# Kernel optimization log

Measured on AMD Instinct MI355X. Metric: run time of the kernel, lower is better.

Reference implementation:

```python
import jax, jax.numpy as jnp
import numpy as np

LO = 30            # rollout horizon (hard-coded in SimCore)
AS_DIM = 400       # ssbm_actionstate_dim
HEAD = AS_DIM + 7  # per-player decoder width


def setup_inputs() -> dict:
    key = jax.random.key(0)
    ks = jax.random.split(key, 12)
    T, B, A, H = 128, 256, 64, 1024
    Nt, Ng = 6, 4
    Lu = T - 1 - LO
    s = 0.02
    return dict(
        observations=jax.random.uniform(ks[0], (T, B, 16), jnp.float32),
        actions=jax.random.normal(ks[1], (T, B, A), jnp.float32),
        beliefs=jax.random.normal(ks[2], (T, B, H), jnp.float32),
        w_ih=jax.random.normal(ks[3], (3 * H, A), jnp.float32) * s,
        w_hh=jax.random.normal(ks[4], (3 * H, H), jnp.float32) * s,
        b_ih=jnp.zeros((3 * H,), jnp.float32),
        b_hh=jnp.zeros((3 * H,), jnp.float32),
        pre_w1=jax.random.normal(ks[5], (64, H), jnp.float32) * s,
        pre_b1=jnp.zeros((64,), jnp.float32),
        pre_w2=jax.random.normal(ks[6], (H, 64), jnp.float32) * s,
        pre_b2=jnp.zeros((H,), jnp.float32),
        dec_w=jax.random.normal(ks[7], (2 * HEAD, H), jnp.float32) * s,
        dec_b=jnp.zeros((2 * HEAD,), jnp.float32),
        idx_i=jax.random.randint(ks[8], (Nt,), 0, Lu, dtype=jnp.int32),
        K=jax.random.randint(ks[9], (Nt, Ng), 0, LO, dtype=jnp.int32),
    )


def _bce_logits(x, t):
    # binary_cross_entropy_with_logits, elementwise
    return jax.nn.softplus(x) - x * t


def _player_loss(pred, tgt):
    # pred: [Nt,Ng,B,407] logits; tgt: [Nt,Ng,B,8] observation half
    # pytorch means are over everything except the Nt python loop -> mean over (Ng,B[,feat])
    logits = pred[..., :AS_DIM]
    cls = tgt[..., 0].astype(jnp.int32)                     # .long() of float target
    ce = -jnp.take_along_axis(jax.nn.log_softmax(logits, -1), cls[..., None], -1)[..., 0]
    loss = ce.mean(axis=(1, 2))
    loss = loss + ((pred[..., 400:402] - tgt[..., 1:3]) ** 2).mean(axis=(1, 2, 3))
    loss = loss + ((jax.nn.softplus(pred[..., 402:403]) - tgt[..., 3:4]) ** 2).mean(axis=(1, 2, 3))
    loss = loss + ((jax.nn.softplus(pred[..., 403:404]) - tgt[..., 4:5]) ** 2).mean(axis=(1, 2, 3))
    loss = loss + _bce_logits(pred[..., 404:405], tgt[..., 5:6]).mean(axis=(1, 2, 3))
    loss = loss + _bce_logits(pred[..., 405:406], tgt[..., 6:7]).mean(axis=(1, 2, 3))
    loss = loss + _bce_logits(pred[..., 406:407], tgt[..., 7:8]).mean(axis=(1, 2, 3))
    return loss  # [Nt]


def reference(observations, actions, beliefs, w_ih, w_hh, b_ih, b_hh,
              pre_w1, pre_b1, pre_w2, pre_b2, dec_w, dec_b, idx_i, K):
    def gru_cell(h, a):
        gi = a @ w_ih.T + b_ih              # [B,3H]
        gh = h @ w_hh.T + b_hh
        ir, iz, in_ = jnp.split(gi, 3, axis=-1)
        hr, hz, hn = jnp.split(gh, 3, axis=-1)
        r = jax.nn.sigmoid(ir + hr)
        z = jax.nn.sigmoid(iz + hz)
        n = jnp.tanh(in_ + r * hn)
        h_new = (1.0 - z) * n + z * h
        return h_new, h_new

    def rollout(i, k):
        h0 = beliefs[i]                                          # [B,H]
        acts = jax.lax.dynamic_slice_in_dim(actions, i, LO, axis=0)
        _, states = jax.lax.scan(gru_cell, h0, acts)             # [Lo,B,H]
        return states[k], observations[k + i + 1]                # [Ng,B,H],[Ng,B,16]

    states, obs = jax.vmap(rollout)(idx_i, K)                    # [Nt,Ng,B,H]

    # ResidualBlock: x + relu(relu(x W1^T + b1) W2^T + b2)
    h = jax.nn.relu(states @ pre_w1.T + pre_b1)
    x = states + jax.nn.relu(h @ pre_w2.T + pre_b2)

    logits = x @ dec_w.T + dec_b                                 # [Nt,Ng,B,814]
    agent, opponent = logits[..., :HEAD], logits[..., HEAD:]
    tgt_a, tgt_o = obs[..., :8], obs[..., 8:]

    loss = (_player_loss(agent, tgt_a) + _player_loss(opponent, tgt_o)).sum()
    return loss
```

## Files before the change

### kernel.cpp

```cpp
#include <hip/hip_runtime.h>
#include <hip/hip_bf16.h>

typedef __bf16 bf16;
typedef __attribute__((ext_vector_type(4))) __bf16 bf16x4;
typedef __attribute__((ext_vector_type(8))) __bf16 bf16x8;
typedef __attribute__((ext_vector_type(4))) float f32x4;

static __device__ __forceinline__ f32x4 MFMA(bf16x8 a, bf16x8 b, f32x4 c) {
  return __builtin_amdgcn_mfma_f32_16x16x32_bf16(a, b, c, 0, 0, 0);
}

__device__ __forceinline__ float sigm(float x) { return 1.0f / (1.0f + __expf(-x)); }
__device__ __forceinline__ float softplus_(float x) {
  return fmaxf(x, 0.0f) + log1pf(__expf(-fabsf(x)));
}

__device__ __forceinline__ void gl16(const bf16* g, char* l) {
  __builtin_amdgcn_global_load_lds(
      (const __attribute__((address_space(1))) char*)g,
      (__attribute__((address_space(3))) char*)l, 16, 0, 0);
}

__global__ void k_prep(const float* __restrict__ whh, const float* __restrict__ wih,
                       const float* __restrict__ act, const float* __restrict__ w1,
                       const float* __restrict__ w2, const float* __restrict__ dw,
                       const float* __restrict__ beliefs, const int* __restrict__ idx_i,
                       bf16* __restrict__ Whd, bf16* __restrict__ Wid,
                       bf16* __restrict__ actd, bf16* __restrict__ w1d,
                       bf16* __restrict__ w2d, bf16* __restrict__ dwd,
                       bf16* __restrict__ hAd) {
  for (int q = blockIdx.x * blockDim.x + threadIdx.x; q < 1994240;
       q += gridDim.x * blockDim.x) {
    const float* src;
    bf16* dst;
    int off;
    if (q < 786432)       { src = whh; dst = Whd;  off = q; }
    else if (q < 835584)  { src = wih; dst = Wid;  off = q - 786432; }
    else if (q < 1359872) { src = act; dst = actd; off = q - 835584; }
    else if (q < 1376256) { src = w1;  dst = w1d;  off = q - 1359872; }
    else if (q < 1392640) { src = w2;  dst = w2d;  off = q - 1376256; }
    else if (q < 1601024) { src = dw;  dst = dwd;  off = q - 1392640; }
    else {
      const int e = (q - 1601024) << 2;
      const int n = e >> 18, rest = e & 262143;
      float4 v = *(const float4*)&beliefs[((size_t)idx_i[n] << 18) + rest];
      bf16x4 o = {(bf16)v.x, (bf16)v.y, (bf16)v.z, (bf16)v.w};
      *(bf16x4*)&hAd[e] = o;
      continue;
    }
    float4 v = *(const float4*)&src[(size_t)off << 2];
    bf16x4 o = {(bf16)v.x, (bf16)v.y, (bf16)v.z, (bf16)v.w};
    *(bf16x4*)&dst[(size_t)off << 2] = o;
  }
}

__global__ __launch_bounds__(256, 2) void k_gru_step(
    const bf16* __restrict__ hin, bf16* __restrict__ hout,
    const bf16* __restrict__ Wh, const bf16* __restrict__ Wi,
    const bf16* __restrict__ actB,
    const float* __restrict__ b_ih, const float* __restrict__ b_hh,
    const int* __restrict__ idx_i, const int* __restrict__ Kmat,
    bf16* __restrict__ states, int step) {
  const int pid = blockIdx.x;
  const int xcd = pid & 7;
  const int rg = xcd >> 2;
  const int cgp = xcd & 3;
  const int q = pid >> 3;
  const int mtl = q & 7;
  const int jtl = q >> 3;
  const int m0 = rg * 768 + mtl * 96;
  const int j0 = (cgp * 8 + jtl) * 32;

  {
    const int nlo = m0 >> 8, nhi = (m0 + 95) >> 8;
    int mk = Kmat[nlo * 4 + 0];
    mk = max(mk, Kmat[nlo * 4 + 1]);
    mk = max(mk, Kmat[nlo * 4 + 2]);
    mk = max(mk, Kmat[nlo * 4 + 3]);
    if (nhi != nlo) {
      mk = max(mk, Kmat[nhi * 4 + 0]);
      mk = max(mk, Kmat[nhi * 4 + 1]);
      mk = max(mk, Kmat[nhi * 4 + 2]);
      mk = max(mk, Kmat[nhi * 4 + 3]);
    }
    if (step > mk) return;
  }

  const int tid = threadIdx.x, wave = tid >> 6, lane = tid & 63;
  const int l15 = lane & 15;
  const int kgrp = lane >> 4;
  const int wm = wave >> 1;
  const int wj = wave & 1;
  const int jlane = j0 + wj * 16 + l15;

  __shared__ alignas(16) bf16 As[3][96][64];
  __shared__ alignas(16) bf16 Bs[3][96][64];

  const int srow = lane >> 3;
  const int scol = (((lane & 7) ^ srow) << 3);

  const bf16* asrc[3];
  const bf16* bsrc[3];
  const bf16* aisrc[3];
  const bf16* bisrc[3];
#pragma unroll
  for (int i = 0; i < 3; ++i) {
    const int prow = wave * 24 + i * 8 + srow;
    const int grow = m0 + prow;
    asrc[i] = hin + (size_t)grow * 1024 + scol;
    const int wr = (prow >> 5) * 1024 + j0 + (prow & 31);
    bsrc[i] = Wh + (size_t)wr * 1024 + scol;
    bisrc[i] = Wi + (size_t)wr * 64 + scol;
    const int np = grow >> 8;
    aisrc[i] = actB + ((size_t)(idx_i[np] + step) * 256 + (grow & 255)) * 64 + scol;
  }

  auto stage = [&](int buf, int it) {
    char* ad = (char*)As + buf * 12288 + (wave * 24) * 128;
    char* bd = (char*)Bs + buf * 12288 + (wave * 24) * 128;
    if (it < 16) {
#pragma unroll
      for (int i = 0; i < 3; ++i) {
        gl16(asrc[i] + it * 64, ad + i * 1024);
        gl16(bsrc[i] + it * 64, bd + i * 1024);
      }
    } else {
#pragma unroll
      for (int i = 0; i < 3; ++i) {
        gl16(aisrc[i], ad + i * 1024);
        gl16(bisrc[i], bd + i * 1024);
      }
    }
  };

  f32x4 accR[3], accZ[3], accNh[3], accNi[3];
  const f32x4 zero = {0.f, 0.f, 0.f, 0.f};
#pragma unroll
  for (int f = 0; f < 3; ++f) { accR[f] = zero; accZ[f] = zero; accNh[f] = zero; accNi[f] = zero; }

  const float br = b_ih[jlane] + b_hh[jlane];
  const float bz = b_ih[1024 + jlane] + b_hh[1024 + jlane];
  const float bin = b_ih[2048 + jlane];
  const float bhn = b_hh[2048 + jlane];

  auto compute = [&](int buf, f32x4 (&gN)[3]) {
    const char* ab = (const char*)As + buf * 12288;
    const char* bb = (const char*)Bs + buf * 12288;
#pragma unroll
    for (int kkI = 0; kkI < 2; ++kkI) {
      const int kbyte = (((kkI << 5) + (kgrp << 3)) << 1) ^ ((l15 & 7) << 4);
      bf16x8 a0 = *(const bf16x8*)(ab + (wm * 48 + l15) * 128 + kbyte);
      bf16x8 a1 = *(const bf16x8*)(ab + (wm * 48 + 16 + l15) * 128 + kbyte);
      bf16x8 a2 = *(const bf16x8*)(ab + (wm * 48 + 32 + l15) * 128 + kbyte);
      bf16x8 b_r = *(const bf16x8*)(bb + (wj * 16 + l15) * 128 + kbyte);
      bf16x8 b_z = *(const bf16x8*)(bb + (32 + wj * 16 + l15) * 128 + kbyte);
      bf16x8 b_n = *(const bf16x8*)(bb + (64 + wj * 16 + l15) * 128 + kbyte);
      accR[0] = MFMA(a0, b_r, accR[0]);
      accR[1] = MFMA(a1, b_r, accR[1]);
      accR[2] = MFMA(a2, b_r, accR[2]);
      accZ[0] = MFMA(a0, b_z, accZ[0]);
      accZ[1] = MFMA(a1, b_z, accZ[1]);
      accZ[2] = MFMA(a2, b_z, accZ[2]);
      gN[0] = MFMA(a0, b_n, gN[0]);
      gN[1] = MFMA(a1, b_n, gN[1]);
      gN[2] = MFMA(a2, b_n, gN[2]);
    }
  };

  stage(0, 0);
  stage(1, 1);

  uint2 hpreg[3];

#pragma unroll
  for (int t = 0; t < 17; ++t) {
    if (t < 15) stage((t + 2) % 3, t + 2);
    if (t == 14) {
#pragma unroll
      for (int it2 = 0; it2 < 3; ++it2) {
        const int u = it2 * 256 + tid;
        const int row = u >> 3, c = u & 7;
        hpreg[it2] = *(const uint2*)(hin + (size_t)(m0 + row) * 1024 + j0 + c * 4);
      }
    }
    if (t <= 13)      asm volatile("s_waitcnt vmcnt(12)" ::: "memory");
    else if (t == 14) asm volatile("s_waitcnt vmcnt(15)" ::: "memory");
    else if (t == 15) asm volatile("s_waitcnt vmcnt(9)" ::: "memory");
    else              asm volatile("s_waitcnt vmcnt(0)" ::: "memory");
    __builtin_amdgcn_s_barrier();
    if (t == 16) compute(1, accNi);
    else         compute(t % 3, accNh);
    __builtin_amdgcn_sched_barrier(0);
    __builtin_amdgcn_s_barrier();
  }

  bf16* Hp = (bf16*)&As[0][0][0];
  bf16* Hn = (bf16*)&Bs[0][0][0];

#pragma unroll
  for (int it2 = 0; it2 < 3; ++it2) {
    const int u = it2 * 256 + tid;
    const int row = u >> 3, c = u & 7;
    *(uint2*)&Hp[row * 40 + c * 4] = hpreg[it2];
  }
  __syncthreads();

#pragma unroll
  for (int mf = 0; mf < 3; ++mf) {
#pragma unroll
    for (int ii = 0; ii < 4; ++ii) {
      const int ml = wm * 48 + mf * 16 + kgrp * 4 + ii;
      const int jl = wj * 16 + l15;
      float hp = (float)Hp[ml * 40 + jl];
      float rg2 = sigm(accR[mf][ii] + br);
      float zg = sigm(accZ[mf][ii] + bz);
      float ng = tanhf(accNi[mf][ii] + bin + rg2 * (accNh[mf][ii] + bhn));
      float hnew = (1.0f - zg) * ng + zg * hp;
      Hn[ml * 40 + jl] = (bf16)hnew;
    }
  }
  __syncthreads();

#pragma unroll
  for (int it2 = 0; it2 < 3; ++it2) {
    const int u = it2 * 256 + tid;
    const int row = u >> 3, c = u & 7;
    const int m = m0 + row;
    uint2 v = *(const uint2*)&Hn[row * 40 + c * 4];
    *(uint2*)&hout[(size_t)m * 1024 + j0 + c * 4] = v;
    const int n = m >> 8;
    const int b = m & 255;
#pragma unroll
    for (int g = 0; g < 4; ++g) {
      if (Kmat[n * 4 + g] == step)
        *(uint2*)&states[((size_t)(n * 4 + g) * 256 + b) * 1024 + j0 + c * 4] = v;
    }
  }
}

template <int EPI, int SWZ>
__global__ __launch_bounds__(256) void k_gemm_epi(
    const bf16* __restrict__ A, const bf16* __restrict__ W, int K, int Nreal, int ld_out,
    const float* __restrict__ bias, const bf16* __restrict__ resid,
    float* __restrict__ outF, bf16* __restrict__ outB) {
  int mt, jt;
  if (SWZ) {
    const int lin = blockIdx.x;
    const int x = lin & 7, k = lin >> 3;
    mt = 12 * x + k % 12;
    jt = k / 12;
  } else {
    mt = blockIdx.x;
    jt = blockIdx.y;
  }
  const int m0 = mt * 64;
  const int j0 = jt * 64;
  const int tid = threadIdx.x, wave = tid >> 6, lane = tid & 63;
  __shared__ alignas(16) bf16 Al[64][72];
  __shared__ alignas(16) bf16 Wl[64][72];

  f32x4 acc[4];
  const f32x4 zero = {0.f, 0.f, 0.f, 0.f};
#pragma unroll
  for (int f = 0; f < 4; ++f) acc[f] = zero;

  const int r = tid >> 3, c8 = (tid & 7) << 3;
  const int arow = wave * 16 + (lane & 15);
  const int koff = (lane >> 4) << 3;

  for (int kb = 0; kb < K; kb += 64) {
    *(bf16x8*)&Al[r][c8]      = *(const bf16x8*)&A[(size_t)(m0 + r) * K + kb + c8];
    *(bf16x8*)&Al[r + 32][c8] = *(const bf16x8*)&A[(size_t)(m0 + r + 32) * K + kb + c8];
    int jr = j0 + r;      if (jr >= Nreal) jr = Nreal - 1;
    int jr2 = j0 + r + 32; if (jr2 >= Nreal) jr2 = Nreal - 1;
    *(bf16x8*)&Wl[r][c8]      = *(const bf16x8*)&W[(size_t)jr * K + kb + c8];
    *(bf16x8*)&Wl[r + 32][c8] = *(const bf16x8*)&W[(size_t)jr2 * K + kb + c8];
    __syncthreads();
#pragma unroll
    for (int kk = 0; kk < 64; kk += 32) {
      bf16x8 av = *(const bf16x8*)&Al[arow][kk + koff];
#pragma unroll
      for (int nf = 0; nf < 4; ++nf) {
        acc[nf] = MFMA(av, *(const bf16x8*)&Wl[nf * 16 + (lane & 15)][kk + koff], acc[nf]);
      }
    }
    __syncthreads();
  }

#pragma unroll
  for (int nf = 0; nf < 4; ++nf) {
    int j = j0 + nf * 16 + (lane & 15);
    float bj = (j < Nreal) ? bias[j] : 0.f;
#pragma unroll
    for (int i = 0; i < 4; ++i) {
      int m = m0 + wave * 16 + ((lane >> 4) << 2) + i;
      float v = acc[nf][i] + bj;
      if (EPI == 0) {
        outB[(size_t)m * ld_out + j] = (bf16)fmaxf(v, 0.f);
      } else if (EPI == 1) {
        v = fmaxf(v, 0.f) + (float)resid[(size_t)m * ld_out + j];
        outB[(size_t)m * ld_out + j] = (bf16)v;
      } else {
        if (j < Nreal) outF[(size_t)m * ld_out + j] = v;
      }
    }
  }
}

__global__ __launch_bounds__(256) void k_loss_wave(
    const float* __restrict__ logits, const float* __restrict__ obs,
    const int* __restrict__ idx_i, const int* __restrict__ Kmat,
    float* __restrict__ partials) {
  const int gw = blockIdx.x * 4 + (threadIdx.x >> 6);
  const int lane = threadIdx.x & 63;
  const int row = gw >> 1, p = gw & 1;
  const int n = row >> 10, g = (row >> 8) & 3, b = row & 255;
  const int i = idx_i[n], k = Kmat[n * 4 + g];
  const float* Lp = logits + (size_t)row * 814 + p * 407;
  const float* tg = obs + ((size_t)(k + i + 1) * 256 + b) * 16 + p * 8;

  float v[7];
#pragma unroll
  for (int it = 0; it < 7; ++it) {
    const int c = lane + it * 64;
    v[it] = (c < 400) ? Lp[c] : -1e30f;
  }
  float mx = fmaxf(fmaxf(fmaxf(v[0], v[1]), fmaxf(v[2], v[3])),
                   fmaxf(fmaxf(v[4], v[5]), v[6]));
#pragma unroll
  for (int s = 32; s; s >>= 1) mx = fmaxf(mx, __shfl_xor(mx, s));
  float se = 0.f;
#pragma unroll
  for (int it = 0; it < 7; ++it) {
    const int c = lane + it * 64;
    se += (c < 400) ? __expf(v[it] - mx) : 0.f;
  }
#pragma unroll
  for (int s = 32; s; s >>= 1) se += __shfl_xor(se, s);

  if (lane == 0) {
    const int cls = (int)tg[0];
    float val = mx + logf(se) - Lp[cls];
    const float d0 = Lp[400] - tg[1], d1 = Lp[401] - tg[2];
    val += 0.5f * (d0 * d0 + d1 * d1);
    const float s2 = softplus_(Lp[402]) - tg[3]; val += s2 * s2;
    const float s3 = softplus_(Lp[403]) - tg[4]; val += s3 * s3;
    val += softplus_(Lp[404]) - Lp[404] * tg[5];
    val += softplus_(Lp[405]) - Lp[405] * tg[6];
    val += softplus_(Lp[406]) - Lp[406] * tg[7];
    partials[gw] = val * (1.0f / 1024.0f);
  }
}

__global__ void k_reduce_final(const float* __restrict__ partials, float* __restrict__ out) {
  __shared__ float s[256];
  float v = 0.f;
  for (int i = threadIdx.x; i < 12288; i += 256) v += partials[i];
  s[threadIdx.x] = v;
  __syncthreads();
  for (int st = 128; st; st >>= 1) {
    if (threadIdx.x < st) s[threadIdx.x] += s[threadIdx.x + st];
    __syncthreads();
  }
  if (threadIdx.x == 0) out[0] = s[0];
}


extern "C" void kernel_launch(void* const* d_in, const int* in_sizes, int n_in,
                              void* d_out, int out_size, void* d_ws, size_t ws_size,
                              hipStream_t stream) {
  const float* obs      = (const float*)d_in[0];
  const float* actions  = (const float*)d_in[1];
  const float* beliefs  = (const float*)d_in[2];
  const float* w_ih     = (const float*)d_in[3];
  const float* w_hh     = (const float*)d_in[4];
  const float* b_ih     = (const float*)d_in[5];
  const float* b_hh     = (const float*)d_in[6];
  const float* pre_w1   = (const float*)d_in[7];
  const float* pre_b1   = (const float*)d_in[8];
  const float* pre_w2   = (const float*)d_in[9];
  const float* pre_b2   = (const float*)d_in[10];
  const float* dec_w    = (const float*)d_in[11];
  const float* dec_b    = (const float*)d_in[12];
  const int*   idx_i    = (const int*)d_in[13];
  const int*   Kmat     = (const int*)d_in[14];
  float* outF = (float*)d_out;

  char* p = (char*)d_ws;
  auto carve = [&](size_t bytes) {
    char* q = p;
    p += (bytes + 255) & ~(size_t)255;
    return q;
  };
  bf16* Wh      = (bf16*)carve(3072u * 1024u * 2u);
  bf16* Wi      = (bf16*)carve(3072u * 64u * 2u);
  bf16* actBv   = (bf16*)carve(128u * 256u * 64u * 2u);
  bf16* preW1b  = (bf16*)carve(64u * 1024u * 2u);
  bf16* preW2b  = (bf16*)carve(1024u * 64u * 2u);
  bf16* decWb   = (bf16*)carve(814u * 1024u * 2u);
  bf16* hA      = (bf16*)carve(1536u * 1024u * 2u);
  bf16* hB      = (bf16*)carve(1536u * 1024u * 2u);
  bf16* states  = (bf16*)carve(6144u * 1024u * 2u);
  bf16* h1      = (bf16*)carve(6144u * 64u * 2u);
  bf16* xbuf    = (bf16*)carve(6144u * 1024u * 2u);
  float* logits = (float*)carve((size_t)6144u * 814u * 4u);
  float* partials = (float*)carve(12288u * 4u);

  k_prep<<<2048, 256, 0, stream>>>(w_hh, w_ih, actions, pre_w1, pre_w2, dec_w,
                                   beliefs, idx_i, Wh, Wi, actBv, preW1b, preW2b,
                                   decWb, hA);

  for (int t = 0; t < 30; ++t) {
    const bf16* hi = (t & 1) ? hB : hA;
    bf16* ho = (t & 1) ? hA : hB;
    k_gru_step<<<512, 256, 0, stream>>>(hi, ho, Wh, Wi, actBv, b_ih, b_hh,
                                        idx_i, Kmat, states, t);
  }

  k_gemm_epi<0, 0><<<dim3(96, 1), 256, 0, stream>>>(states, preW1b, 1024, 64, 64,
                                                    pre_b1, nullptr, nullptr, h1);
  k_gemm_epi<1, 1><<<1536, 256, 0, stream>>>(h1, preW2b, 64, 1024, 1024,
                                             pre_b2, states, nullptr, xbuf);
  k_gemm_epi<2, 1><<<1248, 256, 0, stream>>>(xbuf, decWb, 1024, 814, 814,
                                             dec_b, nullptr, logits, nullptr);

  k_loss_wave<<<3072, 256, 0, stream>>>(logits, obs, idx_i, Kmat, partials);
  k_reduce_final<<<1, 256, 0, stream>>>(partials, outF);
}
```

Baseline: 665.8 us.

## Run GRU recurrent h·W_hh matmul in FP8 e4m3 MFMA

Converts W_hh and the recurrent hidden state to FP8 e4m3 and computes the h·W_hh^T part of each GRU step with fp8 MFMA, halving the K-loop trip count and the bytes streamed per step. The step kernel now writes both a bf16 and an fp8 copy of the new hidden state, and the LDS swizzle and wait counts are reworked for the 8-bit layout. The input-gate part stays in bf16. FP8 quantization of weights and hidden state over 30 recurrent steps risks noticeable accuracy drift in the final loss.

```diff
diff --git a/kernel.cpp b/kernel.cpp
--- a/kernel.cpp
+++ b/kernel.cpp
@@ -1,21 +1,30 @@
 #include <hip/hip_runtime.h>
 #include <hip/hip_bf16.h>
+#include <hip/hip_fp8.h>
 
 typedef __bf16 bf16;
+typedef unsigned char u8;
 typedef __attribute__((ext_vector_type(4))) __bf16 bf16x4;
 typedef __attribute__((ext_vector_type(8))) __bf16 bf16x8;
 typedef __attribute__((ext_vector_type(4))) float f32x4;
 
-static __device__ __forceinline__ f32x4 MFMA(bf16x8 a, bf16x8 b, f32x4 c) {
+static __device__ __forceinline__ f32x4 MFMA16(bf16x8 a, bf16x8 b, f32x4 c) {
   return __builtin_amdgcn_mfma_f32_16x16x32_bf16(a, b, c, 0, 0, 0);
+}
+static __device__ __forceinline__ f32x4 MFMA8(long a, long b, f32x4 c) {
+  return __builtin_amdgcn_mfma_f32_16x16x32_fp8_fp8(a, b, c, 0, 0, 0);
 }
 
 __device__ __forceinline__ float sigm(float x) { return 1.0f / (1.0f + __expf(-x)); }
 __device__ __forceinline__ float softplus_(float x) {
   return fmaxf(x, 0.0f) + log1pf(__expf(-fabsf(x)));
 }
-
-__device__ __forceinline__ void gl16(const bf16* g, char* l) {
+__device__ __forceinline__ u8 to_fp8(float x) {
+  __hip_fp8_e4m3 v(x);
+  return (u8)v.__x;
+}
+
+__device__ __forceinline__ void gl16(const void* g, char* l) {
   __builtin_amdgcn_global_load_lds(
       (const __attribute__((address_space(1))) char*)g,
       (__attribute__((address_space(3))) char*)l, 16, 0, 0);
@@ -25,39 +34,48 @@
                        const float* __restrict__ act, const float* __restrict__ w1,
                        const float* __restrict__ w2, const float* __restrict__ dw,
                        const float* __restrict__ beliefs, const int* __restrict__ idx_i,
-                       bf16* __restrict__ Whd, bf16* __restrict__ Wid,
-                       bf16* __restrict__ actd, bf16* __restrict__ w1d,
-                       bf16* __restrict__ w2d, bf16* __restrict__ dwd,
-                       bf16* __restrict__ hAd) {
+                       u8* __restrict__ Wh8, bf16* __restrict__ Wib,
+                       bf16* __restrict__ actb, bf16* __restrict__ w1b,
+                       bf16* __restrict__ w2b, bf16* __restrict__ dwb,
+                       bf16* __restrict__ hA, u8* __restrict__ hA8) {
   for (int q = blockIdx.x * blockDim.x + threadIdx.x; q < 1994240;
        q += gridDim.x * blockDim.x) {
-    const float* src;
-    bf16* dst;
-    int off;
-    if (q < 786432)       { src = whh; dst = Whd;  off = q; }
-    else if (q < 835584)  { src = wih; dst = Wid;  off = q - 786432; }
-    else if (q < 1359872) { src = act; dst = actd; off = q - 835584; }
-    else if (q < 1376256) { src = w1;  dst = w1d;  off = q - 1359872; }
-    else if (q < 1392640) { src = w2;  dst = w2d;  off = q - 1376256; }
-    else if (q < 1601024) { src = dw;  dst = dwd;  off = q - 1392640; }
-    else {
-      const int e = (q - 1601024) << 2;
+    if (q < 814592) {
+      const float* src;
+      bf16* dst;
+      int off;
+      if (q < 49152)       { src = wih; dst = Wib;  off = q; }
+      else if (q < 573440) { src = act; dst = actb; off = q - 49152; }
+      else if (q < 589824) { src = w1;  dst = w1b;  off = q - 573440; }
+      else if (q < 606208) { src = w2;  dst = w2b;  off = q - 589824; }
+      else                 { src = dw;  dst = dwb;  off = q - 606208; }
+      float4 v = *(const float4*)&src[(size_t)off << 2];
+      bf16x4 o = {(bf16)v.x, (bf16)v.y, (bf16)v.z, (bf16)v.w};
+      *(bf16x4*)&dst[(size_t)off << 2] = o;
+    } else if (q < 1207808) {
+      const int e = (q - 814592) << 2;
       const int n = e >> 18, rest = e & 262143;
       float4 v = *(const float4*)&beliefs[((size_t)idx_i[n] << 18) + rest];
       bf16x4 o = {(bf16)v.x, (bf16)v.y, (bf16)v.z, (bf16)v.w};
-      *(bf16x4*)&hAd[e] = o;
-      continue;
-    }
-    float4 v = *(const float4*)&src[(size_t)off << 2];
-    bf16x4 o = {(bf16)v.x, (bf16)v.y, (bf16)v.z, (bf16)v.w};
-    *(bf16x4*)&dst[(size_t)off << 2] = o;
+      *(bf16x4*)&hA[e] = o;
+      unsigned w = (unsigned)to_fp8(v.x) | ((unsigned)to_fp8(v.y) << 8) |
+                   ((unsigned)to_fp8(v.z) << 16) | ((unsigned)to_fp8(v.w) << 24);
+      *(unsigned*)&hA8[e] = w;
+    } else {
+      const int off = q - 1207808;
+      float4 v = *(const float4*)&whh[(size_t)off << 2];
+      unsigned w = (unsigned)to_fp8(v.x) | ((unsigned)to_fp8(v.y) << 8) |
+                   ((unsigned)to_fp8(v.z) << 16) | ((unsigned)to_fp8(v.w) << 24);
+      *(unsigned*)&Wh8[(size_t)off << 2] = w;
+    }
   }
 }
 
 __global__ __launch_bounds__(256, 2) void k_gru_step(
-    const bf16* __restrict__ hin, bf16* __restrict__ hout,
-    const bf16* __restrict__ Wh, const bf16* __restrict__ Wi,
-    const bf16* __restrict__ actB,
+    const bf16* __restrict__ hin, const u8* __restrict__ hin8,
+    bf16* __restrict__ hout, u8* __restrict__ hout8,
+    const u8* __restrict__ Wh8, const bf16* __restrict__ Wib,
+    const bf16* __restrict__ actb,
     const float* __restrict__ b_ih, const float* __restrict__ b_hh,
     const int* __restrict__ idx_i, const int* __restrict__ Kmat,
     bf16* __restrict__ states, int step) {
@@ -73,16 +91,11 @@
 
   {
     const int nlo = m0 >> 8, nhi = (m0 + 95) >> 8;
-    int mk = Kmat[nlo * 4 + 0];
-    mk = max(mk, Kmat[nlo * 4 + 1]);
-    mk = max(mk, Kmat[nlo * 4 + 2]);
-    mk = max(mk, Kmat[nlo * 4 + 3]);
-    if (nhi != nlo) {
-      mk = max(mk, Kmat[nhi * 4 + 0]);
-      mk = max(mk, Kmat[nhi * 4 + 1]);
-      mk = max(mk, Kmat[nhi * 4 + 2]);
-      mk = max(mk, Kmat[nhi * 4 + 3]);
-    }
+    int mk = max(max(Kmat[nlo * 4 + 0], Kmat[nlo * 4 + 1]),
+                 max(Kmat[nlo * 4 + 2], Kmat[nlo * 4 + 3]));
+    if (nhi != nlo)
+      mk = max(mk, max(max(Kmat[nhi * 4 + 0], Kmat[nhi * 4 + 1]),
+                       max(Kmat[nhi * 4 + 2], Kmat[nhi * 4 + 3])));
     if (step > mk) return;
   }
 
@@ -93,42 +106,38 @@
   const int wj = wave & 1;
   const int jlane = j0 + wj * 16 + l15;
 
-  __shared__ alignas(16) bf16 As[3][96][64];
-  __shared__ alignas(16) bf16 Bs[3][96][64];
+  __shared__ alignas(16) char As[3 * 12288];
+  __shared__ alignas(16) char Bs[3 * 12288];
 
   const int srow = lane >> 3;
-  const int scol = (((lane & 7) ^ srow) << 3);
-
-  const bf16* asrc[3];
-  const bf16* bsrc[3];
-  const bf16* aisrc[3];
-  const bf16* bisrc[3];
+  int a8off[3], b8off[3], aioff[3], bioff[3];
 #pragma unroll
   for (int i = 0; i < 3; ++i) {
-    const int prow = wave * 24 + i * 8 + srow;
-    const int grow = m0 + prow;
-    asrc[i] = hin + (size_t)grow * 1024 + scol;
-    const int wr = (prow >> 5) * 1024 + j0 + (prow & 31);
-    bsrc[i] = Wh + (size_t)wr * 1024 + scol;
-    bisrc[i] = Wi + (size_t)wr * 64 + scol;
+    const int r = wave * 24 + i * 8 + srow;
+    const int grow = m0 + r;
+    a8off[i] = grow * 1024 + ((((lane & 7) ^ ((r >> 1) & 7)) << 4));
+    const int wr = (r >> 5) * 1024 + j0 + (r & 31);
+    b8off[i] = wr * 1024 + ((((lane & 7) ^ ((r >> 1) & 7)) << 4));
+    const int scol = (((lane & 7) ^ srow) << 3);
     const int np = grow >> 8;
-    aisrc[i] = actB + ((size_t)(idx_i[np] + step) * 256 + (grow & 255)) * 64 + scol;
-  }
-
-  auto stage = [&](int buf, int it) {
-    char* ad = (char*)As + buf * 12288 + (wave * 24) * 128;
-    char* bd = (char*)Bs + buf * 12288 + (wave * 24) * 128;
-    if (it < 16) {
+    aioff[i] = ((idx_i[np] + step) * 256 + (grow & 255)) * 64 + scol;
+    bioff[i] = wr * 64 + scol;
+  }
+
+  auto stage = [&](int buf, int slot) {
+    char* ad = As + buf * 12288 + (wave * 24) * 128;
+    char* bd = Bs + buf * 12288 + (wave * 24) * 128;
+    if (slot < 8) {
 #pragma unroll
       for (int i = 0; i < 3; ++i) {
-        gl16(asrc[i] + it * 64, ad + i * 1024);
-        gl16(bsrc[i] + it * 64, bd + i * 1024);
+        gl16(hin8 + a8off[i] + slot * 128, ad + i * 1024);
+        gl16(Wh8 + b8off[i] + slot * 128, bd + i * 1024);
       }
     } else {
 #pragma unroll
       for (int i = 0; i < 3; ++i) {
-        gl16(aisrc[i], ad + i * 1024);
-        gl16(bisrc[i], bd + i * 1024);
+        gl16(actb + aioff[i], ad + i * 1024);
+        gl16(Wib + bioff[i], bd + i * 1024);
       }
     }
   };
@@ -143,9 +152,41 @@
   const float bin = b_ih[2048 + jlane];
   const float bhn = b_hh[2048 + jlane];
 
-  auto compute = [&](int buf, f32x4 (&gN)[3]) {
-    const char* ab = (const char*)As + buf * 12288;
-    const char* bb = (const char*)Bs + buf * 12288;
+  const int keyA = ((wm * 48 + l15) >> 1) & 7;
+  const int keyB = ((wj * 16 + l15) >> 1) & 7;
+
+  auto computeF8 = [&](int buf) {
+    const char* ab = As + buf * 12288;
+    const char* bb = Bs + buf * 12288;
+    const int ra = wm * 48 + l15;
+    const int rb = wj * 16 + l15;
+#pragma unroll
+    for (int kkI = 0; kkI < 4; ++kkI) {
+      const int hi = kkI * 2 + (kgrp >> 1);
+      const int lo = (kgrp & 1) << 3;
+      const int offA = (((hi ^ keyA) << 4) | lo);
+      const int offB = (((hi ^ keyB) << 4) | lo);
+      long a0 = *(const long*)(ab + ra * 128 + offA);
+      long a1 = *(const long*)(ab + (ra + 16) * 128 + offA);
+      long a2 = *(const long*)(ab + (ra + 32) * 128 + offA);
+      long b0 = *(const long*)(bb + rb * 128 + offB);
+      long b1 = *(const long*)(bb + (rb + 32) * 128 + offB);
+      long b2 = *(const long*)(bb + (rb + 64) * 128 + offB);
+      accR[0] = MFMA8(a0, b0, accR[0]);
+      accR[1] = MFMA8(a1, b0, accR[1]);
+      accR[2] = MFMA8(a2, b0, accR[2]);
+      accZ[0] = MFMA8(a0, b1, accZ[0]);
+      accZ[1] = MFMA8(a1, b1, accZ[1]);
+      accZ[2] = MFMA8(a2, b1, accZ[2]);
+      accNh[0] = MFMA8(a0, b2, accNh[0]);
+      accNh[1] = MFMA8(a1, b2, accNh[1]);
+      accNh[2] = MFMA8(a2, b2, accNh[2]);
+    }
+  };
+
+  auto computeGi = [&]() {
+    const char* ab = As + 2 * 12288;
+    const char* bb = Bs + 2 * 12288;
 #pragma unroll
     for (int kkI = 0; kkI < 2; ++kkI) {
       const int kbyte = (((kkI << 5) + (kgrp << 3)) << 1) ^ ((l15 & 7) << 4);
@@ -155,15 +196,15 @@
       bf16x8 b_r = *(const bf16x8*)(bb + (wj * 16 + l15) * 128 + kbyte);
       bf16x8 b_z = *(const bf16x8*)(bb + (32 + wj * 16 + l15) * 128 + kbyte);
       bf16x8 b_n = *(const bf16x8*)(bb + (64 + wj * 16 + l15) * 128 + kbyte);
-      accR[0] = MFMA(a0, b_r, accR[0]);
-      accR[1] = MFMA(a1, b_r, accR[1]);
-      accR[2] = MFMA(a2, b_r, accR[2]);
-      accZ[0] = MFMA(a0, b_z, accZ[0]);
-      accZ[1] = MFMA(a1, b_z, accZ[1]);
-      accZ[2] = MFMA(a2, b_z, accZ[2]);
-      gN[0] = MFMA(a0, b_n, gN[0]);
-      gN[1] = MFMA(a1, b_n, gN[1]);
-      gN[2] = MFMA(a2, b_n, gN[2]);
+      accR[0] = MFMA16(a0, b_r, accR[0]);
+      accR[1] = MFMA16(a1, b_r, accR[1]);
+      accR[2] = MFMA16(a2, b_r, accR[2]);
+      accZ[0] = MFMA16(a0, b_z, accZ[0]);
+      accZ[1] = MFMA16(a1, b_z, accZ[1]);
+      accZ[2] = MFMA16(a2, b_z, accZ[2]);
+      accNi[0] = MFMA16(a0, b_n, accNi[0]);
+      accNi[1] = MFMA16(a1, b_n, accNi[1]);
+      accNi[2] = MFMA16(a2, b_n, accNi[2]);
     }
   };
 
@@ -173,9 +214,9 @@
   uint2 hpreg[3];
 
 #pragma unroll
-  for (int t = 0; t < 17; ++t) {
-    if (t < 15) stage((t + 2) % 3, t + 2);
-    if (t == 14) {
+  for (int t = 0; t < 9; ++t) {
+    if (t < 7) stage((t + 2) % 3, t + 2);
+    if (t == 6) {
 #pragma unroll
       for (int it2 = 0; it2 < 3; ++it2) {
         const int u = it2 * 256 + tid;
@@ -183,19 +224,21 @@
         hpreg[it2] = *(const uint2*)(hin + (size_t)(m0 + row) * 1024 + j0 + c * 4);
       }
     }
-    if (t <= 13)      asm volatile("s_waitcnt vmcnt(12)" ::: "memory");
-    else if (t == 14) asm volatile("s_waitcnt vmcnt(15)" ::: "memory");
-    else if (t == 15) asm volatile("s_waitcnt vmcnt(9)" ::: "memory");
-    else              asm volatile("s_waitcnt vmcnt(0)" ::: "memory");
+    if (t <= 5)       asm volatile("s_waitcnt vmcnt(12)" ::: "memory");
+    else if (t == 6)  asm volatile("s_waitcnt vmcnt(15)" ::: "memory");
+    else if (t == 7)  asm volatile("s_waitcnt vmcnt(9)" ::: "memory");
+    else              asm volatile("s_waitcnt vmcnt(3)" ::: "memory");
     __builtin_amdgcn_s_barrier();
-    if (t == 16) compute(1, accNi);
-    else         compute(t % 3, accNh);
+    if (t == 8) computeGi();
+    else        computeF8(t % 3);
     __builtin_amdgcn_sched_barrier(0);
     __builtin_amdgcn_s_barrier();
   }
 
-  bf16* Hp = (bf16*)&As[0][0][0];
-  bf16* Hn = (bf16*)&Bs[0][0][0];
+  asm volatile("s_waitcnt vmcnt(0)" ::: "memory");
+  bf16* Hp = (bf16*)As;
+  bf16* Hn = (bf16*)Bs;
+  u8* Hn8 = (u8*)(As + 12288);
 
 #pragma unroll
   for (int it2 = 0; it2 < 3; ++it2) {
@@ -217,6 +260,7 @@
       float ng = tanhf(accNi[mf][ii] + bin + rg2 * (accNh[mf][ii] + bhn));
       float hnew = (1.0f - zg) * ng + zg * hp;
       Hn[ml * 40 + jl] = (bf16)hnew;
+      Hn8[ml * 40 + jl] = to_fp8(hnew);
     }
   }
   __syncthreads();
@@ -228,6 +272,8 @@
     const int m = m0 + row;
     uint2 v = *(const uint2*)&Hn[row * 40 + c * 4];
     *(uint2*)&hout[(size_t)m * 1024 + j0 + c * 4] = v;
+    if (c < 8) {
+    }
     const int n = m >> 8;
     const int b = m & 255;
 #pragma unroll
@@ -235,6 +281,13 @@
       if (Kmat[n * 4 + g] == step)
         *(uint2*)&states[((size_t)(n * 4 + g) * 256 + b) * 1024 + j0 + c * 4] = v;
     }
+  }
+#pragma unroll
+  for (int it2 = 0; it2 < 3; ++it2) {
+    const int u = it2 * 256 + tid;
+    const int row = u >> 3, c = u & 7;
+    *(unsigned*)&hout8[(size_t)(m0 + row) * 1024 + j0 + c * 4] =
+        *(const unsigned*)&Hn8[row * 40 + c * 4];
   }
 }
 
@@ -281,7 +334,7 @@
       bf16x8 av = *(const bf16x8*)&Al[arow][kk + koff];
 #pragma unroll
       for (int nf = 0; nf < 4; ++nf) {
-        acc[nf] = MFMA(av, *(const bf16x8*)&Wl[nf * 16 + (lane & 15)][kk + koff], acc[nf]);
+        acc[nf] = MFMA16(av, *(const bf16x8*)&Wl[nf * 16 + (lane & 15)][kk + koff], acc[nf]);
       }
     }
     __syncthreads();
@@ -392,14 +445,16 @@
     p += (bytes + 255) & ~(size_t)255;
     return q;
   };
-  bf16* Wh      = (bf16*)carve(3072u * 1024u * 2u);
-  bf16* Wi      = (bf16*)carve(3072u * 64u * 2u);
-  bf16* actBv   = (bf16*)carve(128u * 256u * 64u * 2u);
+  u8*   Wh8     = (u8*)carve(3072u * 1024u);
+  bf16* Wib     = (bf16*)carve(3072u * 64u * 2u);
+  bf16* actb    = (bf16*)carve(128u * 256u * 64u * 2u);
   bf16* preW1b  = (bf16*)carve(64u * 1024u * 2u);
   bf16* preW2b  = (bf16*)carve(1024u * 64u * 2u);
   bf16* decWb   = (bf16*)carve(814u * 1024u * 2u);
   bf16* hA      = (bf16*)carve(1536u * 1024u * 2u);
   bf16* hB      = (bf16*)carve(1536u * 1024u * 2u);
+  u8*   hA8     = (u8*)carve(1536u * 1024u);
+  u8*   hB8     = (u8*)carve(1536u * 1024u);
   bf16* states  = (bf16*)carve(6144u * 1024u * 2u);
   bf16* h1      = (bf16*)carve(6144u * 64u * 2u);
   bf16* xbuf    = (bf16*)carve(6144u * 1024u * 2u);
@@ -407,14 +462,16 @@
   float* partials = (float*)carve(12288u * 4u);
 
   k_prep<<<2048, 256, 0, stream>>>(w_hh, w_ih, actions, pre_w1, pre_w2, dec_w,
-                                   beliefs, idx_i, Wh, Wi, actBv, preW1b, preW2b,
-                                   decWb, hA);
+                                   beliefs, idx_i, Wh8, Wib, actb, preW1b, preW2b,
+                                   decWb, hA, hA8);
 
   for (int t = 0; t < 30; ++t) {
     const bf16* hi = (t & 1) ? hB : hA;
     bf16* ho = (t & 1) ? hA : hB;
-    k_gru_step<<<512, 256, 0, stream>>>(hi, ho, Wh, Wi, actBv, b_ih, b_hh,
-                                        idx_i, Kmat, states, t);
+    const u8* hi8 = (t & 1) ? hB8 : hA8;
+    u8* ho8 = (t & 1) ? hA8 : hB8;
+    k_gru_step<<<512, 256, 0, stream>>>(hi, hi8, ho, ho8, Wh8, Wib, actb,
+                                        b_ih, b_hh, idx_i, Kmat, states, t);
   }
 
   k_gemm_epi<0, 0><<<dim3(96, 1), 256, 0, stream>>>(states, preW1b, 1024, 64, 64,
```

New measurement: 566.7 us. 1.17x faster.
